# Kernel tuning notes

Hardware: AMD Instinct MI355X
Metric: run time of the kernel (lower is better)

## Reference

```python
import jax, jax.numpy as jnp
import numpy as np

VOCAB = 32000
EMB = 512
HEADS = 8
HEAD_DIM = EMB // HEADS
MLP = 2048
LAYERS = 6
KERNEL_EPS = 1e-3  # performer generalized-attention kernel_epsilon
LN_EPS = 1e-6


def sinusoidal_pos_emb(seq_len, dim):
    pos = np.arange(seq_len)[:, None].astype(np.float32)
    div = np.exp(np.arange(0, dim, 2).astype(np.float32) * (-np.log(10000.0) / dim))
    pe = np.zeros((seq_len, dim), dtype=np.float32)
    pe[:, 0::2] = np.sin(pos * div)
    pe[:, 1::2] = np.cos(pos * div)
    return jnp.asarray(pe)


def setup_inputs() -> dict:
    key = jax.random.key(0)
    ks = jax.random.split(key, 16)
    B, S = 4, 4096
    s_emb = 1.0 / np.sqrt(EMB)
    s_head = 1.0 / np.sqrt(HEAD_DIM)
    s_mlp = 1.0 / np.sqrt(MLP)
    return {
        'tokens': jax.random.randint(ks[0], (B, S), 0, VOCAB),
        'embed': jax.random.normal(ks[1], (VOCAB, EMB), jnp.float32) * s_emb,
        'Wq': jax.random.normal(ks[2], (LAYERS, EMB, HEADS, HEAD_DIM), jnp.float32) * s_emb,
        'Wk': jax.random.normal(ks[3], (LAYERS, EMB, HEADS, HEAD_DIM), jnp.float32) * s_emb,
        'Wv': jax.random.normal(ks[4], (LAYERS, EMB, HEADS, HEAD_DIM), jnp.float32) * s_emb,
        'Wo': jax.random.normal(ks[5], (LAYERS, HEADS, HEAD_DIM, EMB), jnp.float32) * s_head,
        'ln1_s': jnp.ones((LAYERS, EMB), jnp.float32),
        'ln1_b': jnp.zeros((LAYERS, EMB), jnp.float32),
        'W1': jax.random.normal(ks[6], (LAYERS, EMB, MLP), jnp.float32) * s_emb,
        'b1': jnp.zeros((LAYERS, MLP), jnp.float32),
        'W2': jax.random.normal(ks[7], (LAYERS, MLP, EMB), jnp.float32) * s_mlp,
        'b2': jnp.zeros((LAYERS, EMB), jnp.float32),
        'ln2_s': jnp.ones((LAYERS, EMB), jnp.float32),
        'ln2_b': jnp.zeros((LAYERS, EMB), jnp.float32),
        'lnf_s': jnp.ones((EMB,), jnp.float32),
        'lnf_b': jnp.zeros((EMB,), jnp.float32),
    }


def layer_norm(x, s, b):
    mu = jnp.mean(x, axis=-1, keepdims=True)
    var = jnp.mean(jnp.square(x - mu), axis=-1, keepdims=True)
    return (x - mu) * jax.lax.rsqrt(var + LN_EPS) * s + b


def favor_generalized_attention(x, Wq, Wk, Wv, Wo):
    # Performer generalized attention, deterministic ReLU feature map,
    # renormalized (bidirectional): O(S * m * d) linear attention.
    q = jnp.einsum('bsd,dhf->bshf', x, Wq)
    k = jnp.einsum('bsd,dhf->bshf', x, Wk)
    v = jnp.einsum('bsd,dhf->bshf', x, Wv)
    pq = jax.nn.relu(q) + KERNEL_EPS  # phi(q): [B,S,H,F]
    pk = jax.nn.relu(k) + KERNEL_EPS  # phi(k)
    kv = jnp.einsum('bshf,bshe->bhfe', pk, v)          # [B,H,F,E]
    num = jnp.einsum('bshf,bhfe->bshe', pq, kv)        # numerator
    den = jnp.einsum('bshf,bhf->bsh', pq, pk.sum(axis=1))  # renormalizer
    attn = num / den[..., None]
    return jnp.einsum('bshe,hed->bsd', attn, Wo)


def reference(tokens, embed, Wq, Wk, Wv, Wo, ln1_s, ln1_b, W1, b1, W2, b2,
              ln2_s, ln2_b, lnf_s, lnf_b):
    B, S = tokens.shape
    x = embed[tokens] + sinusoidal_pos_emb(S, EMB)[None, :, :]
    for l in range(LAYERS):
        h = layer_norm(x, ln1_s[l], ln1_b[l])
        x = x + favor_generalized_attention(h, Wq[l], Wk[l], Wv[l], Wo[l])
        h = layer_norm(x, ln2_s[l], ln2_b[l])
        h = jax.nn.gelu(h @ W1[l] + b1[l]) @ W2[l] + b2[l]
        x = x + h
    return layer_norm(x, lnf_s, lnf_b)
```

## Files before the change

kernel.cpp:

```cpp
#include <hip/hip_runtime.h>

typedef float f32x4 __attribute__((ext_vector_type(4)));
typedef __bf16 bf16x8 __attribute__((ext_vector_type(8)));

#define NROWS 16384
#define SEQ   4096
#define EMBD  512
#define MLPD  2048

__device__ inline float gelu_tanh(float x) {
    float t = 0.7978845608028654f * (x + 0.044715f * x * x * x);
    float e = __expf(2.f * t);
    float th = 1.f - 2.f / (1.f + e);
    return 0.5f * x * (1.f + th);
}

#define GLOAD16(gp, lp)                                                        \
    __builtin_amdgcn_global_load_lds(                                          \
        (const __attribute__((address_space(1))) void*)(gp),                   \
        (__attribute__((address_space(3))) void*)(lp), 16, 0, 0)

__global__ void pos_kernel(float* __restrict__ pos) {
    int i = blockIdx.x * 256 + threadIdx.x;
    int s = i >> 8, j = i & 255;
    float div = __expf((float)j * (-2.f * 9.210340371976184f / 512.f));
    float a = (float)s * div;
    pos[(size_t)s * 512 + 2 * j]     = sinf(a);
    pos[(size_t)s * 512 + 2 * j + 1] = cosf(a);
}

__global__ void embed_kernel(const int* __restrict__ tokens,
                             const float* __restrict__ embed,
                             const float* __restrict__ pos,
                             float* __restrict__ x) {
    int row = blockIdx.x;
    int t = threadIdx.x;
    int s = row & (SEQ - 1);
    int tok = tokens[row];
    f32x4 e = *(const f32x4*)(embed + (size_t)tok * 512 + t * 4);
    f32x4 p = *(const f32x4*)(pos + (size_t)s * 512 + t * 4);
    e += p;
    *(f32x4*)(x + (size_t)row * 512 + t * 4) = e;
}

__global__ void transpose_bf16(const float* __restrict__ in, __bf16* __restrict__ out,
                               int K, int N, size_t in_lstride, size_t out_lstride) {
    __shared__ float tile[32][33];
    in  += (size_t)blockIdx.z * in_lstride;
    out += (size_t)blockIdx.z * out_lstride;
    int n0 = blockIdx.x * 32, k0 = blockIdx.y * 32;
    int tx = threadIdx.x, ty = threadIdx.y;
    #pragma unroll
    for (int i = 0; i < 32; i += 8)
        tile[ty + i][tx] = in[(size_t)(k0 + ty + i) * N + n0 + tx];
    __syncthreads();
    #pragma unroll
    for (int i = 0; i < 32; i += 8)
        out[(size_t)(n0 + ty + i) * K + k0 + tx] = (__bf16)tile[tx][ty + i];
}

template<int OUTBF>
__global__ __launch_bounds__(256) void ln_kernel(
    const float* __restrict__ x, const float* __restrict__ gamma,
    const float* __restrict__ beta, __bf16* __restrict__ outb,
    float* __restrict__ outf) {
    int lane = threadIdx.x & 63;
    size_t row = (size_t)blockIdx.x * 4 + (threadIdx.x >> 6);
    const float* xr = x + row * 512 + lane * 8;
    f32x4 v0 = *(const f32x4*)xr;
    f32x4 v1 = *(const f32x4*)(xr + 4);
    float sum = (v0[0] + v0[1]) + (v0[2] + v0[3]) + (v1[0] + v1[1]) + (v1[2] + v1[3]);
    #pragma unroll
    for (int off = 32; off; off >>= 1) sum += __shfl_xor(sum, off);
    float mu = sum * (1.f / 512.f);
    float vs = 0.f;
    #pragma unroll
    for (int j = 0; j < 4; j++) {
        float d0 = v0[j] - mu; vs += d0 * d0;
        float d1 = v1[j] - mu; vs += d1 * d1;
    }
    #pragma unroll
    for (int off = 32; off; off >>= 1) vs += __shfl_xor(vs, off);
    float inv = rsqrtf(vs * (1.f / 512.f) + 1e-6f);
    const float* gp = gamma + lane * 8;
    const float* bp = beta + lane * 8;
    f32x4 g0 = *(const f32x4*)gp, g1 = *(const f32x4*)(gp + 4);
    f32x4 bb0 = *(const f32x4*)bp, bb1 = *(const f32x4*)(bp + 4);
    float o[8];
    #pragma unroll
    for (int j = 0; j < 4; j++) {
        o[j]     = (v0[j] - mu) * inv * g0[j] + bb0[j];
        o[4 + j] = (v1[j] - mu) * inv * g1[j] + bb1[j];
    }
    if (OUTBF) {
        bf16x8 ov;
        #pragma unroll
        for (int j = 0; j < 8; j++) ov[j] = (__bf16)o[j];
        *(bf16x8*)(outb + row * 512 + lane * 8) = ov;
    } else {
        f32x4 o0 = {o[0], o[1], o[2], o[3]};
        f32x4 o1 = {o[4], o[5], o[6], o[7]};
        *(f32x4*)(outf + row * 512 + lane * 8) = o0;
        *(f32x4*)(outf + row * 512 + lane * 8 + 4) = o1;
    }
}

template<int EPI, int K, int BM>
__global__ __launch_bounds__(256, 4) void gemm_bt(
    const __bf16* __restrict__ A, const __bf16* __restrict__ BT,
    float* __restrict__ Cf, __bf16* __restrict__ Cb,
    const float* __restrict__ bias, int N, int nbn) {
    constexpr int NT = K / 32;
    constexpr int AL = BM / 64;
    constexpr int LPS = AL + 2;
    constexpr int NREP = (BM == 128) ? 4 : 2;
    __shared__ __align__(16) __bf16 Asm[3][BM * 32];
    __shared__ __align__(16) __bf16 Bsm[3][128 * 32];
    const int t = threadIdx.x;
    const int lane = t & 63;
    const int wave = t >> 6;
    const int wr = (BM == 128) ? (wave >> 1) : 0;
    const int wc = (BM == 128) ? (wave & 1) : wave;
    const int nblk = gridDim.x;
    const int q = nblk >> 3, r = nblk & 7;
    const int xcd = blockIdx.x & 7, loc = blockIdx.x >> 3;
    const int swz = (xcd < r ? xcd * (q + 1) : r * (q + 1) + (xcd - r) * q) + loc;
    const int m0 = (swz / nbn) * BM, n0 = (swz % nbn) * 128;
    const int fr = lane & 15, fc = lane >> 4;

    const __bf16* Aps[AL];
    const __bf16* Bps[2];
    int aslot[AL], bslot[2];
    #pragma unroll
    for (int j = 0; j < AL; j++) {
        int slot = t + 256 * j;
        int row = slot >> 2, cp = slot & 3;
        int sc = cp ^ ((row >> 1) & 3);
        Aps[j] = A + (size_t)(m0 + row) * K + sc * 8;
        aslot[j] = slot * 8;
    }
    #pragma unroll
    for (int j = 0; j < 2; j++) {
        int slot = t + 256 * j;
        int row = slot >> 2, cp = slot & 3;
        int sc = cp ^ ((row >> 1) & 3);
        Bps[j] = BT + (size_t)(n0 + row) * K + sc * 8;
        bslot[j] = slot * 8;
    }

    f32x4 acc[4][NREP];
    #pragma unroll
    for (int m = 0; m < 4; m++)
        #pragma unroll
        for (int n = 0; n < NREP; n++)
            acc[m][n] = (f32x4){0.f, 0.f, 0.f, 0.f};

    auto stage = [&](int koff, __bf16* Ad, __bf16* Bd) {
        #pragma unroll
        for (int j = 0; j < AL; j++) GLOAD16(Aps[j] + koff, Ad + aslot[j]);
        #pragma unroll
        for (int j = 0; j < 2; j++) GLOAD16(Bps[j] + koff, Bd + bslot[j]);
    };

    stage(0, Asm[0], Bsm[0]);
    stage(32, Asm[1], Bsm[1]);

    for (int s = 0; s < NT; s++) {
        if (s + 1 < NT) {
            asm volatile("s_waitcnt vmcnt(%0)" :: "i"(LPS) : "memory");
        } else {
            asm volatile("s_waitcnt vmcnt(0)" ::: "memory");
        }
        __builtin_amdgcn_s_barrier();
        if (s + 2 < NT) {
            int sl = (s + 2) % 3;
            stage((s + 2) * 32, Asm[sl], Bsm[sl]);
        }
        const __bf16* Ac = Asm[s % 3];
        const __bf16* Bc = Bsm[s % 3];

        bf16x8 af[4], bfr[NREP];
        #pragma unroll
        for (int m = 0; m < 4; m++) {
            int ra = ((BM == 128) ? wr * 64 : 0) + m * 16 + fr;
            af[m] = *(const bf16x8*)(Ac + ra * 32 + ((fc ^ ((ra >> 1) & 3)) << 3));
        }
        #pragma unroll
        for (int n = 0; n < NREP; n++) {
            int rb = wc * (16 * NREP) + n * 16 + fr;
            bfr[n] = *(const bf16x8*)(Bc + rb * 32 + ((fc ^ ((rb >> 1) & 3)) << 3));
        }
        __builtin_amdgcn_s_setprio(1);
        #pragma unroll
        for (int m = 0; m < 4; m++)
            #pragma unroll
            for (int n = 0; n < NREP; n++)
                acc[m][n] = __builtin_amdgcn_mfma_f32_16x16x32_bf16(af[m], bfr[n], acc[m][n], 0, 0, 0);
        __builtin_amdgcn_s_setprio(0);
    }

    const int cr = (lane >> 4) * 4;
    const int cc = lane & 15;
    #pragma unroll
    for (int m = 0; m < 4; m++) {
        #pragma unroll
        for (int n = 0; n < NREP; n++) {
            #pragma unroll
            for (int r2 = 0; r2 < 4; r2++) {
                int grow = m0 + ((BM == 128) ? wr * 64 : 0) + m * 16 + cr + r2;
                int gcol = n0 + wc * (16 * NREP) + n * 16 + cc;
                size_t idx = (size_t)grow * N + gcol;
                float val = acc[m][n][r2];
                if (EPI == 1) {
                    if (gcol < 1024) val = fmaxf(val, 0.f) + 1e-3f;
                    Cb[idx] = (__bf16)val;
                } else if (EPI == 2) {
                    Cf[idx] += val;
                } else if (EPI == 3) {
                    val += bias[gcol];
                    Cb[idx] = (__bf16)gelu_tanh(val);
                } else if (EPI == 4) {
                    Cf[idx] += val + bias[gcol];
                } else {
                    Cf[idx] = val;
                }
            }
        }
    }
}

__global__ __launch_bounds__(256) void kv_partial(const __bf16* __restrict__ qkvb,
                                                  float* __restrict__ part) {
    int bh = blockIdx.x;
    int chunk = blockIdx.y;
    int b = bh >> 3, hh = bh & 7;
    int t = threadIdx.x;
    int f = t & 63, eg = t >> 6;
    size_t base = ((size_t)b * SEQ + (size_t)chunk * 128) * 1536;
    const __bf16* kcol = qkvb + base + 512 + hh * 64 + f;
    const __bf16* vrow = qkvb + base + 1024 + hh * 64 + eg * 16;
    float psum = 0.f;
    f32x4 a0 = {0.f,0.f,0.f,0.f}, a1 = a0, a2 = a0, a3 = a0;
    for (int s = 0; s < 128; s++) {
        size_t o = (size_t)s * 1536;
        float pk = (float)kcol[o];
        psum += pk;
        bf16x8 w0 = *(const bf16x8*)(vrow + o);
        bf16x8 w1 = *(const bf16x8*)(vrow + o + 8);
        #pragma unroll
        for (int j = 0; j < 4; j++) {
            a0[j] += (float)w0[j]     * pk;
            a1[j] += (float)w0[4 + j] * pk;
            a2[j] += (float)w1[j]     * pk;
            a3[j] += (float)w1[4 + j] * pk;
        }
    }
    float* dst = part + ((size_t)chunk * 32 + bh) * 4160 + (size_t)f * 65 + eg * 16;
    #pragma unroll
    for (int j = 0; j < 4; j++) { dst[j] = a0[j]; dst[4+j] = a1[j]; dst[8+j] = a2[j]; dst[12+j] = a3[j]; }
    if (eg == 0) dst[64] = psum;
}

__global__ void kv_reduce(const float* __restrict__ part, float* __restrict__ kvfin) {
    int i = blockIdx.x * 256 + threadIdx.x;
    if (i >= 32 * 4160) return;
    float s = 0.f;
    #pragma unroll 8
    for (int c = 0; c < 32; c++) s += part[(size_t)c * (32 * 4160) + i];
    kvfin[i] = s;
}

__global__ __launch_bounds__(256) void num_attn(const __bf16* __restrict__ qkvb,
                                                const float* __restrict__ kvfin,
                                                __bf16* __restrict__ attn) {
    __shared__ __bf16 kvb[64][86];
    int bh = blockIdx.x, chunk = blockIdx.y;
    int b = bh >> 3, hh = bh & 7;
    const float* src = kvfin + (size_t)bh * 4160;
    int t = threadIdx.x;
    for (int i = t; i < 4096; i += 256) {
        int f = i >> 6, e = i & 63;
        kvb[f][e] = (__bf16)src[f * 65 + e];
    }
    if (t < 64) {
        kvb[t][64] = (__bf16)src[t * 65 + 64];
        #pragma unroll
        for (int e = 65; e < 80; e++) kvb[t][e] = (__bf16)0.f;
    }
    const int lane = t & 63, w = t >> 6;
    const int fr = lane & 15, fc = lane >> 4;
    size_t rowbase = (size_t)b * SEQ + (size_t)chunk * 128 + w * 32;
    bf16x8 a[2][2];
    #pragma unroll
    for (int rt = 0; rt < 2; rt++)
        #pragma unroll
        for (int ks = 0; ks < 2; ks++)
            a[rt][ks] = *(const bf16x8*)(qkvb + (rowbase + rt * 16 + fr) * 1536 + hh * 64 + ks * 32 + fc * 8);
    __syncthreads();
    bf16x8 bfrag[5][2];
    #pragma unroll
    for (int n = 0; n < 5; n++)
        #pragma unroll
        for (int ks = 0; ks < 2; ks++) {
            bf16x8 bv;
            #pragma unroll
            for (int j = 0; j < 8; j++) bv[j] = kvb[ks * 32 + fc * 8 + j][n * 16 + fr];
            bfrag[n][ks] = bv;
        }
    f32x4 acc[2][5];
    #pragma unroll
    for (int rt = 0; rt < 2; rt++)
        #pragma unroll
        for (int n = 0; n < 5; n++)
            acc[rt][n] = (f32x4){0.f, 0.f, 0.f, 0.f};
    #pragma unroll
    for (int ks = 0; ks < 2; ks++)
        #pragma unroll
        for (int rt = 0; rt < 2; rt++)
            #pragma unroll
            for (int n = 0; n < 5; n++)
                acc[rt][n] = __builtin_amdgcn_mfma_f32_16x16x32_bf16(a[rt][ks], bfrag[n][ks], acc[rt][n], 0, 0, 0);
    const int cr = (lane >> 4) * 4, cc = lane & 15;
    #pragma unroll
    for (int rt = 0; rt < 2; rt++) {
        float rdv[4];
        #pragma unroll
        for (int r2 = 0; r2 < 4; r2++)
            rdv[r2] = 1.f / __shfl(acc[rt][4][r2], lane & 48);
        #pragma unroll
        for (int r2 = 0; r2 < 4; r2++) {
            int lr = w * 32 + rt * 16 + cr + r2;
            size_t grow = (size_t)b * SEQ + (size_t)chunk * 128 + lr;
            #pragma unroll
            for (int n = 0; n < 4; n++)
                attn[grow * 512 + hh * 64 + n * 16 + cc] = (__bf16)(acc[rt][n][r2] * rdv[r2]);
        }
    }
}

extern "C" void kernel_launch(void* const* d_in, const int* in_sizes, int n_in,
                              void* d_out, int out_size, void* d_ws, size_t ws_size,
                              hipStream_t stream) {
    const int*   tokens = (const int*)d_in[0];
    const float* embed  = (const float*)d_in[1];
    const float* Wq     = (const float*)d_in[2];
    const float* Wk     = (const float*)d_in[3];
    const float* Wv     = (const float*)d_in[4];
    const float* Wo     = (const float*)d_in[5];
    const float* ln1_s  = (const float*)d_in[6];
    const float* ln1_b  = (const float*)d_in[7];
    const float* W1     = (const float*)d_in[8];
    const float* b1     = (const float*)d_in[9];
    const float* W2     = (const float*)d_in[10];
    const float* b2     = (const float*)d_in[11];
    const float* ln2_s  = (const float*)d_in[12];
    const float* ln2_b  = (const float*)d_in[13];
    const float* lnf_s  = (const float*)d_in[14];
    const float* lnf_b  = (const float*)d_in[15];
    float* out = (float*)d_out;

    float* ws = (float*)d_ws;
    size_t off = 0;
    float* pos = ws;               off += 2097152;
    float* x   = ws + off;         off += 8388608;
    __bf16* h    = (__bf16*)(ws + off); off += 4194304;
    __bf16* attn = (__bf16*)(ws + off); off += 4194304;
    __bf16* qkvb = (__bf16*)(ws + off);
    __bf16* hid  = (__bf16*)(ws + off); off += 16777216;
    float* kvpart = ws + off;      off += 32 * 32 * 4160;
    float* kvfin  = ws + off;      off += 32 * 4160;
    __bf16* wbuf  = (__bf16*)(ws + off);

    pos_kernel<<<4096, 256, 0, stream>>>(pos);
    transpose_bf16<<<dim3(16, 16, 6), dim3(32, 8), 0, stream>>>(Wq, wbuf,          512, 512,  262144, 3145728);
    transpose_bf16<<<dim3(16, 16, 6), dim3(32, 8), 0, stream>>>(Wk, wbuf + 262144, 512, 512,  262144, 3145728);
    transpose_bf16<<<dim3(16, 16, 6), dim3(32, 8), 0, stream>>>(Wv, wbuf + 524288, 512, 512,  262144, 3145728);
    transpose_bf16<<<dim3(16, 16, 6), dim3(32, 8), 0, stream>>>(Wo, wbuf + 786432, 512, 512,  262144, 3145728);
    transpose_bf16<<<dim3(64, 16, 6), dim3(32, 8), 0, stream>>>(W1, wbuf + 1048576, 512, 2048, 1048576, 3145728);
    transpose_bf16<<<dim3(16, 64, 6), dim3(32, 8), 0, stream>>>(W2, wbuf + 2097152, 2048, 512, 1048576, 3145728);
    embed_kernel<<<16384, 128, 0, stream>>>(tokens, embed, pos, x);

    for (int l = 0; l < 6; l++) {
        const __bf16* wl = wbuf + (size_t)l * 3145728;
        ln_kernel<1><<<4096, 256, 0, stream>>>(x, ln1_s + l * 512, ln1_b + l * 512, h, nullptr);
        gemm_bt<1, 512, 128><<<1536, 256, 0, stream>>>(h, wl, nullptr, qkvb, nullptr, 1536, 12);
        kv_partial<<<dim3(32, 32), 256, 0, stream>>>(qkvb, kvpart);
        kv_reduce<<<520, 256, 0, stream>>>(kvpart, kvfin);
        num_attn<<<dim3(32, 32), 256, 0, stream>>>(qkvb, kvfin, attn);
        gemm_bt<2, 512, 64><<<1024, 256, 0, stream>>>(attn, wl + 786432, x, nullptr, nullptr, 512, 4);
        ln_kernel<1><<<4096, 256, 0, stream>>>(x, ln2_s + l * 512, ln2_b + l * 512, h, nullptr);
        gemm_bt<3, 512, 128><<<2048, 256, 0, stream>>>(h, wl + 1048576, nullptr, hid, b1 + (size_t)l * 2048, 2048, 16);
        gemm_bt<4, 2048, 64><<<1024, 256, 0, stream>>>(hid, wl + 2097152, x, nullptr, b2 + (size_t)l * 512, 512, 4);
    }
    ln_kernel<0><<<4096, 256, 0, stream>>>(x, lnf_s, lnf_b, nullptr, out);
}
```

Measured before the change: 1.744 ms.

## Fuse residual add and LayerNorm into full-row output-projection GEMMs

Adds a gemm_ln kernel in which each 512-thread block computes a full 64x512 output row tile, adds the bias and residual, computes LayerNorm statistics across waves through shared memory, and writes both the updated residual and the bf16 normalized activations. The embedding kernel also gets the first LayerNorm fused in. Together these remove all standalone ln_kernel launches and their extra passes over x. The trade-off is that the Wo and W2 GEMMs now launch only 256 blocks with large B tiles and double buffering. That lowers parallelism across the CUs, and the variance is computed as E[x^2]-mu^2, which is less numerically robust.

```diff
diff --git a/kernel.cpp b/kernel.cpp
--- a/kernel.cpp
+++ b/kernel.cpp
@@ -29,18 +29,45 @@
     pos[(size_t)s * 512 + 2 * j + 1] = cosf(a);
 }
 
-__global__ void embed_kernel(const int* __restrict__ tokens,
-                             const float* __restrict__ embed,
-                             const float* __restrict__ pos,
-                             float* __restrict__ x) {
-    int row = blockIdx.x;
-    int t = threadIdx.x;
-    int s = row & (SEQ - 1);
+__global__ __launch_bounds__(256) void embed_ln(
+    const int* __restrict__ tokens, const float* __restrict__ embed,
+    const float* __restrict__ pos, const float* __restrict__ gamma,
+    const float* __restrict__ beta, float* __restrict__ x,
+    __bf16* __restrict__ h) {
+    int lane = threadIdx.x & 63;
+    size_t row = (size_t)blockIdx.x * 4 + (threadIdx.x >> 6);
+    int s = (int)(row & (SEQ - 1));
     int tok = tokens[row];
-    f32x4 e = *(const f32x4*)(embed + (size_t)tok * 512 + t * 4);
-    f32x4 p = *(const f32x4*)(pos + (size_t)s * 512 + t * 4);
-    e += p;
-    *(f32x4*)(x + (size_t)row * 512 + t * 4) = e;
+    const float* ep = embed + (size_t)tok * 512 + lane * 8;
+    const float* pp = pos + (size_t)s * 512 + lane * 8;
+    f32x4 v0 = *(const f32x4*)ep + *(const f32x4*)pp;
+    f32x4 v1 = *(const f32x4*)(ep + 4) + *(const f32x4*)(pp + 4);
+    *(f32x4*)(x + row * 512 + lane * 8) = v0;
+    *(f32x4*)(x + row * 512 + lane * 8 + 4) = v1;
+    float sum = (v0[0] + v0[1]) + (v0[2] + v0[3]) + (v1[0] + v1[1]) + (v1[2] + v1[3]);
+    #pragma unroll
+    for (int off = 32; off; off >>= 1) sum += __shfl_xor(sum, off);
+    float mu = sum * (1.f / 512.f);
+    float vs = 0.f;
+    #pragma unroll
+    for (int j = 0; j < 4; j++) {
+        float d0 = v0[j] - mu; vs += d0 * d0;
+        float d1 = v1[j] - mu; vs += d1 * d1;
+    }
+    #pragma unroll
+    for (int off = 32; off; off >>= 1) vs += __shfl_xor(vs, off);
+    float inv = rsqrtf(vs * (1.f / 512.f) + 1e-6f);
+    const float* gp = gamma + lane * 8;
+    const float* bp = beta + lane * 8;
+    f32x4 g0 = *(const f32x4*)gp, g1 = *(const f32x4*)(gp + 4);
+    f32x4 bb0 = *(const f32x4*)bp, bb1 = *(const f32x4*)(bp + 4);
+    bf16x8 ov;
+    #pragma unroll
+    for (int j = 0; j < 4; j++) {
+        ov[j]     = (__bf16)((v0[j] - mu) * inv * g0[j] + bb0[j]);
+        ov[4 + j] = (__bf16)((v1[j] - mu) * inv * g1[j] + bb1[j]);
+    }
+    *(bf16x8*)(h + row * 512 + lane * 8) = ov;
 }
 
 __global__ void transpose_bf16(const float* __restrict__ in, __bf16* __restrict__ out,
@@ -57,52 +84,6 @@
     #pragma unroll
     for (int i = 0; i < 32; i += 8)
         out[(size_t)(n0 + ty + i) * K + k0 + tx] = (__bf16)tile[tx][ty + i];
-}
-
-template<int OUTBF>
-__global__ __launch_bounds__(256) void ln_kernel(
-    const float* __restrict__ x, const float* __restrict__ gamma,
-    const float* __restrict__ beta, __bf16* __restrict__ outb,
-    float* __restrict__ outf) {
-    int lane = threadIdx.x & 63;
-    size_t row = (size_t)blockIdx.x * 4 + (threadIdx.x >> 6);
-    const float* xr = x + row * 512 + lane * 8;
-    f32x4 v0 = *(const f32x4*)xr;
-    f32x4 v1 = *(const f32x4*)(xr + 4);
-    float sum = (v0[0] + v0[1]) + (v0[2] + v0[3]) + (v1[0] + v1[1]) + (v1[2] + v1[3]);
-    #pragma unroll
-    for (int off = 32; off; off >>= 1) sum += __shfl_xor(sum, off);
-    float mu = sum * (1.f / 512.f);
-    float vs = 0.f;
-    #pragma unroll
-    for (int j = 0; j < 4; j++) {
-        float d0 = v0[j] - mu; vs += d0 * d0;
-        float d1 = v1[j] - mu; vs += d1 * d1;
-    }
-    #pragma unroll
-    for (int off = 32; off; off >>= 1) vs += __shfl_xor(vs, off);
-    float inv = rsqrtf(vs * (1.f / 512.f) + 1e-6f);
-    const float* gp = gamma + lane * 8;
-    const float* bp = beta + lane * 8;
-    f32x4 g0 = *(const f32x4*)gp, g1 = *(const f32x4*)(gp + 4);
-    f32x4 bb0 = *(const f32x4*)bp, bb1 = *(const f32x4*)(bp + 4);
-    float o[8];
-    #pragma unroll
-    for (int j = 0; j < 4; j++) {
-        o[j]     = (v0[j] - mu) * inv * g0[j] + bb0[j];
-        o[4 + j] = (v1[j] - mu) * inv * g1[j] + bb1[j];
-    }
-    if (OUTBF) {
-        bf16x8 ov;
-        #pragma unroll
-        for (int j = 0; j < 8; j++) ov[j] = (__bf16)o[j];
-        *(bf16x8*)(outb + row * 512 + lane * 8) = ov;
-    } else {
-        f32x4 o0 = {o[0], o[1], o[2], o[3]};
-        f32x4 o1 = {o[4], o[5], o[6], o[7]};
-        *(f32x4*)(outf + row * 512 + lane * 8) = o0;
-        *(f32x4*)(outf + row * 512 + lane * 8 + 4) = o1;
-    }
 }
 
 template<int EPI, int K, int BM>
@@ -214,15 +195,171 @@
                 if (EPI == 1) {
                     if (gcol < 1024) val = fmaxf(val, 0.f) + 1e-3f;
                     Cb[idx] = (__bf16)val;
-                } else if (EPI == 2) {
-                    Cf[idx] += val;
                 } else if (EPI == 3) {
                     val += bias[gcol];
                     Cb[idx] = (__bf16)gelu_tanh(val);
-                } else if (EPI == 4) {
-                    Cf[idx] += val + bias[gcol];
                 } else {
                     Cf[idx] = val;
+                }
+            }
+        }
+    }
+}
+
+template<int HASB, int K, int FINAL>
+__global__ __launch_bounds__(512) void gemm_ln(
+    const __bf16* __restrict__ A, const __bf16* __restrict__ BT,
+    const float* __restrict__ bias, float* __restrict__ x,
+    const float* __restrict__ gamma, const float* __restrict__ beta,
+    __bf16* __restrict__ hout, float* __restrict__ fout) {
+    constexpr int NT = K / 32;
+    __shared__ __align__(16) __bf16 Asm[2][64 * 32];
+    __shared__ __align__(16) __bf16 Bsm[2][512 * 32];
+    __shared__ float sums[64][8][2];
+    __shared__ float rowstat[64][2];
+    const int t = threadIdx.x;
+    const int lane = t & 63;
+    const int wave = t >> 6;
+    const int wc = wave;
+    const int m0 = blockIdx.x * 64;
+    const int fr = lane & 15, fc = lane >> 4;
+
+    const __bf16* Ap = A;
+    int aslot = 0;
+    if (t < 256) {
+        int row = t >> 2, cp = t & 3;
+        int sc = cp ^ ((row >> 1) & 3);
+        Ap = A + (size_t)(m0 + row) * K + sc * 8;
+        aslot = t * 8;
+    }
+    const __bf16* Bps[4];
+    int bslot[4];
+    #pragma unroll
+    for (int j = 0; j < 4; j++) {
+        int slot = t + 512 * j;
+        int row = slot >> 2, cp = slot & 3;
+        int sc = cp ^ ((row >> 1) & 3);
+        Bps[j] = BT + (size_t)row * K + sc * 8;
+        bslot[j] = slot * 8;
+    }
+    auto stage = [&](int koff, __bf16* Ad, __bf16* Bd) {
+        if (t < 256) GLOAD16(Ap + koff, Ad + aslot);
+        #pragma unroll
+        for (int j = 0; j < 4; j++) GLOAD16(Bps[j] + koff, Bd + bslot[j]);
+    };
+
+    f32x4 acc[4][4];
+    #pragma unroll
+    for (int m = 0; m < 4; m++)
+        #pragma unroll
+        for (int n = 0; n < 4; n++)
+            acc[m][n] = (f32x4){0.f, 0.f, 0.f, 0.f};
+
+    stage(0, Asm[0], Bsm[0]);
+    int cur = 0;
+    for (int s = 0; s < NT; s++) {
+        if (s + 1 < NT) {
+            stage((s + 1) * 32, Asm[cur ^ 1], Bsm[cur ^ 1]);
+            if (wave < 4) asm volatile("s_waitcnt vmcnt(5)" ::: "memory");
+            else          asm volatile("s_waitcnt vmcnt(4)" ::: "memory");
+        } else {
+            asm volatile("s_waitcnt vmcnt(0)" ::: "memory");
+        }
+        __builtin_amdgcn_s_barrier();
+        const __bf16* Ac = Asm[cur];
+        const __bf16* Bc = Bsm[cur];
+        bf16x8 af[4], bfr[4];
+        #pragma unroll
+        for (int m = 0; m < 4; m++) {
+            int ra = m * 16 + fr;
+            af[m] = *(const bf16x8*)(Ac + ra * 32 + ((fc ^ ((ra >> 1) & 3)) << 3));
+        }
+        #pragma unroll
+        for (int n = 0; n < 4; n++) {
+            int rb = wc * 64 + n * 16 + fr;
+            bfr[n] = *(const bf16x8*)(Bc + rb * 32 + ((fc ^ ((rb >> 1) & 3)) << 3));
+        }
+        __builtin_amdgcn_s_setprio(1);
+        #pragma unroll
+        for (int m = 0; m < 4; m++)
+            #pragma unroll
+            for (int n = 0; n < 4; n++)
+                acc[m][n] = __builtin_amdgcn_mfma_f32_16x16x32_bf16(af[m], bfr[n], acc[m][n], 0, 0, 0);
+        __builtin_amdgcn_s_setprio(0);
+        __builtin_amdgcn_s_barrier();
+        cur ^= 1;
+    }
+
+    const int cr = (lane >> 4) * 4;
+    const int cc = lane & 15;
+    float bia[4], gam[4], bet[4];
+    #pragma unroll
+    for (int n = 0; n < 4; n++) {
+        int gcol = wc * 64 + n * 16 + cc;
+        bia[n] = HASB ? bias[gcol] : 0.f;
+        gam[n] = gamma[gcol];
+        bet[n] = beta[gcol];
+    }
+    float xn[4][4][4];
+    #pragma unroll
+    for (int m = 0; m < 4; m++) {
+        #pragma unroll
+        for (int r2 = 0; r2 < 4; r2++) {
+            int grow = m0 + m * 16 + cr + r2;
+            #pragma unroll
+            for (int n = 0; n < 4; n++) {
+                int gcol = wc * 64 + n * 16 + cc;
+                xn[m][n][r2] = acc[m][n][r2] + bia[n] + x[(size_t)grow * 512 + gcol];
+            }
+        }
+    }
+    #pragma unroll
+    for (int m = 0; m < 4; m++) {
+        #pragma unroll
+        for (int r2 = 0; r2 < 4; r2++) {
+            float s1 = 0.f, q1 = 0.f;
+            #pragma unroll
+            for (int n = 0; n < 4; n++) { float v = xn[m][n][r2]; s1 += v; q1 += v * v; }
+            #pragma unroll
+            for (int off = 1; off <= 8; off <<= 1) {
+                s1 += __shfl_xor(s1, off);
+                q1 += __shfl_xor(q1, off);
+            }
+            if (cc == 0) {
+                int rl = m * 16 + cr + r2;
+                sums[rl][wave][0] = s1;
+                sums[rl][wave][1] = q1;
+            }
+        }
+    }
+    __syncthreads();
+    if (t < 64) {
+        float S = 0.f, Q = 0.f;
+        #pragma unroll
+        for (int w = 0; w < 8; w++) { S += sums[t][w][0]; Q += sums[t][w][1]; }
+        float mu = S * (1.f / 512.f);
+        float var = Q * (1.f / 512.f) - mu * mu;
+        rowstat[t][0] = mu;
+        rowstat[t][1] = rsqrtf(var + 1e-6f);
+    }
+    __syncthreads();
+    #pragma unroll
+    for (int m = 0; m < 4; m++) {
+        #pragma unroll
+        for (int r2 = 0; r2 < 4; r2++) {
+            int rl = m * 16 + cr + r2;
+            int grow = m0 + rl;
+            float mu = rowstat[rl][0], inv = rowstat[rl][1];
+            #pragma unroll
+            for (int n = 0; n < 4; n++) {
+                int gcol = wc * 64 + n * 16 + cc;
+                float v = xn[m][n][r2];
+                float hv = (v - mu) * inv * gam[n] + bet[n];
+                if (!FINAL) {
+                    x[(size_t)grow * 512 + gcol] = v;
+                    hout[(size_t)grow * 512 + gcol] = (__bf16)hv;
+                } else {
+                    fout[(size_t)grow * 512 + gcol] = hv;
                 }
             }
         }
@@ -378,19 +515,23 @@
     transpose_bf16<<<dim3(16, 16, 6), dim3(32, 8), 0, stream>>>(Wo, wbuf + 786432, 512, 512,  262144, 3145728);
     transpose_bf16<<<dim3(64, 16, 6), dim3(32, 8), 0, stream>>>(W1, wbuf + 1048576, 512, 2048, 1048576, 3145728);
     transpose_bf16<<<dim3(16, 64, 6), dim3(32, 8), 0, stream>>>(W2, wbuf + 2097152, 2048, 512, 1048576, 3145728);
-    embed_kernel<<<16384, 128, 0, stream>>>(tokens, embed, pos, x);
+    embed_ln<<<4096, 256, 0, stream>>>(tokens, embed, pos, ln1_s, ln1_b, x, h);
 
     for (int l = 0; l < 6; l++) {
         const __bf16* wl = wbuf + (size_t)l * 3145728;
-        ln_kernel<1><<<4096, 256, 0, stream>>>(x, ln1_s + l * 512, ln1_b + l * 512, h, nullptr);
         gemm_bt<1, 512, 128><<<1536, 256, 0, stream>>>(h, wl, nullptr, qkvb, nullptr, 1536, 12);
         kv_partial<<<dim3(32, 32), 256, 0, stream>>>(qkvb, kvpart);
         kv_reduce<<<520, 256, 0, stream>>>(kvpart, kvfin);
         num_attn<<<dim3(32, 32), 256, 0, stream>>>(qkvb, kvfin, attn);
-        gemm_bt<2, 512, 64><<<1024, 256, 0, stream>>>(attn, wl + 786432, x, nullptr, nullptr, 512, 4);
-        ln_kernel<1><<<4096, 256, 0, stream>>>(x, ln2_s + l * 512, ln2_b + l * 512, h, nullptr);
+        gemm_ln<0, 512, 0><<<256, 512, 0, stream>>>(attn, wl + 786432, nullptr, x,
+                                                    ln2_s + l * 512, ln2_b + l * 512, h, nullptr);
         gemm_bt<3, 512, 128><<<2048, 256, 0, stream>>>(h, wl + 1048576, nullptr, hid, b1 + (size_t)l * 2048, 2048, 16);
-        gemm_bt<4, 2048, 64><<<1024, 256, 0, stream>>>(hid, wl + 2097152, x, nullptr, b2 + (size_t)l * 512, 512, 4);
-    }
-    ln_kernel<0><<<4096, 256, 0, stream>>>(x, lnf_s, lnf_b, nullptr, out);
-}
+        if (l < 5) {
+            gemm_ln<1, 2048, 0><<<256, 512, 0, stream>>>(hid, wl + 2097152, b2 + (size_t)l * 512, x,
+                                                         ln1_s + (l + 1) * 512, ln1_b + (l + 1) * 512, h, nullptr);
+        } else {
+            gemm_ln<1, 2048, 1><<<256, 512, 0, stream>>>(hid, wl + 2097152, b2 + (size_t)l * 512, x,
+                                                         lnf_s, lnf_b, nullptr, out);
+        }
+    }
+}
```

New measurement: 1.781 ms. 2.1% more time.
